# Performance work log

Hardware: AMD Instinct MI355X
Metric: run time of the kernel (lower is better)

The kernel has to match this reference:

```python
import jax, jax.numpy as jnp
import numpy as np

B, L, D = 1, 1024, 1024
NL = 4            # n_layers
N = 16            # d_state
DI = 2 * D        # d_inner (expand=2)
DTR = (D + 15) // 16  # dt_rank = ceil(d_model/16) = 64
K = 4             # depthwise conv kernel size
EPS = 1e-5


def setup_inputs() -> dict:
    key = jax.random.key(0)
    ks = jax.random.split(key, 8)
    s = lambda k, shp, sc: jax.random.normal(k, shp, jnp.float32) * sc
    x = s(ks[0], (B, L, D), 1.0)
    norm_w = jnp.ones((NL, D), jnp.float32)
    in_w = s(ks[1], (NL, 2 * DI, D), D ** -0.5)          # in_proj (no bias)
    conv_w = s(ks[2], (NL, DI, K), 0.5)                   # depthwise conv1d weight
    conv_b = s(ks[3], (NL, DI), 0.02)                     # conv1d bias
    xproj_w = s(ks[4], (NL, DTR + 2 * N, DI), DI ** -0.5) # x_proj (no bias)
    dt_w = s(ks[5], (NL, DI, DTR), DTR ** -0.5)           # dt_proj weight
    dt_b = jnp.full((NL, DI), 0.1, jnp.float32)           # dt_proj bias (positive-ish delta)
    A_log = jnp.log(jnp.tile(jnp.arange(1, N + 1, dtype=jnp.float32), (NL, DI, 1)))  # [NL, DI, N]
    D_skip = jnp.ones((NL, DI), jnp.float32)
    out_w = s(ks[6], (NL, D, DI), DI ** -0.5)             # out_proj (no bias)
    return dict(x=x, norm_w=norm_w, in_w=in_w, conv_w=conv_w, conv_b=conv_b,
                xproj_w=xproj_w, dt_w=dt_w, dt_b=dt_b, A_log=A_log,
                D_skip=D_skip, out_w=out_w)


def _rmsnorm(x, w):
    return x * jax.lax.rsqrt(jnp.mean(x * x, axis=-1, keepdims=True) + EPS) * w


def _causal_depthwise_conv(u, w, b):
    # u: [B, L, DI], w: [DI, K], b: [DI]; causal (left pad K-1)
    up = jnp.pad(u, ((0, 0), (K - 1, 0), (0, 0)))
    y = b
    for k in range(K):
        y = y + up[:, k:k + L, :] * w[:, k]
    return y


def _selective_scan(dA, dBu, C):
    # dA, dBu: [B, L, DI, N]; C: [B, L, N]
    def step(h, inp):
        a, bu, c = inp
        h = a * h + bu                       # [B, DI, N]
        y = jnp.einsum('bdn,bn->bd', h, c)   # [B, DI]
        return h, y
    h0 = jnp.zeros((dA.shape[0], DI, N), dA.dtype)
    _, ys = jax.lax.scan(step, h0, (dA.transpose(1, 0, 2, 3),
                                    dBu.transpose(1, 0, 2, 3),
                                    C.transpose(1, 0, 2)))
    return ys.transpose(1, 0, 2)             # [B, L, DI]


def _mamba_block(x, p):
    norm_w, in_w, conv_w, conv_b, xproj_w, dt_w, dt_b, A_log, D_skip, out_w = p
    xn = _rmsnorm(x, norm_w)
    xz = jnp.einsum('bld,ed->ble', xn, in_w)             # [B, L, 2*DI]
    u, z = jnp.split(xz, 2, axis=-1)
    u = jax.nn.silu(_causal_depthwise_conv(u, conv_w, conv_b))
    x_dbl = jnp.einsum('bld,ed->ble', u, xproj_w)        # [B, L, DTR+2N]
    dt_r, Bt, Ct = jnp.split(x_dbl, [DTR, DTR + N], axis=-1)
    delta = jax.nn.softplus(jnp.einsum('blr,dr->bld', dt_r, dt_w) + dt_b)  # [B, L, DI]
    A = -jnp.exp(A_log)                                  # [DI, N]
    dA = jnp.exp(delta[..., None] * A)                   # [B, L, DI, N]
    dBu = delta[..., None] * Bt[:, :, None, :] * u[..., None]
    y = _selective_scan(dA, dBu, Ct) + u * D_skip        # [B, L, DI]
    y = y * jax.nn.silu(z)
    return x + jnp.einsum('ble,de->bld', y, out_w)       # residual


def reference(x, norm_w, in_w, conv_w, conv_b, xproj_w, dt_w, dt_b, A_log, D_skip, out_w):
    params = (norm_w, in_w, conv_w, conv_b, xproj_w, dt_w, dt_b, A_log, D_skip, out_w)
    out, _ = jax.lax.scan(lambda h, p: (_mamba_block(h, p), None), x, params)
    return out
```

## Files before the change

### kernel.cpp

```cpp
#include <hip/hip_runtime.h>
#include <hip/hip_bf16.h>
#include <stdint.h>

#define L 1024
#define D 1024
#define NLAYER 4
#define NSTATE 16
#define DI 2048
#define DTR 64
#define KCONV 4
#define XD 96
#define NC 64
#define CT 16
#define KSPLIT 8

typedef __attribute__((ext_vector_type(8))) short short8;
typedef __attribute__((ext_vector_type(4))) float floatx4;

__device__ __forceinline__ float siluf(float x) { return x / (1.f + __expf(-x)); }

__device__ __forceinline__ unsigned short f2bf(float x) {
    __hip_bfloat16 b = __float2bfloat16(x);
    return *reinterpret_cast<unsigned short*>(&b);
}

#ifndef __has_builtin
#define __has_builtin(x) 0
#endif
#if __has_builtin(__builtin_amdgcn_global_load_lds)
#define HAVE_GLD 1
#define GLD(gp, lp) __builtin_amdgcn_global_load_lds(                                  \
    (const __attribute__((address_space(1))) void*)(gp),                               \
    (__attribute__((address_space(3))) void*)(lp), 16, 0, 0)
#endif

#define N_IN4  1048576
#define N_XP4  49152
#define N_DT4  32768
#define N_OUT4 524288
#define N_CVT4 (N_IN4 + N_XP4 + N_DT4 + N_OUT4)

__global__ __launch_bounds__(256) void cvt_layer_kernel(
    const float* __restrict__ in_w, const float* __restrict__ xp_w,
    const float* __restrict__ dt_w, const float* __restrict__ out_w,
    __hip_bfloat16* __restrict__ in_bf, __hip_bfloat16* __restrict__ xp_bf,
    __hip_bfloat16* __restrict__ dt_bf, __hip_bfloat16* __restrict__ out_bf) {
    int i = blockIdx.x * 256 + threadIdx.x;
    if (i >= N_CVT4) return;
    const float* src;
    __hip_bfloat16* dst;
    int off;
    if (i < N_IN4) { src = in_w; dst = in_bf; off = i; }
    else if (i < N_IN4 + N_XP4) { src = xp_w; dst = xp_bf; off = i - N_IN4; }
    else if (i < N_IN4 + N_XP4 + N_DT4) { src = dt_w; dst = dt_bf; off = i - N_IN4 - N_XP4; }
    else { src = out_w; dst = out_bf; off = i - N_IN4 - N_XP4 - N_DT4; }
    float4 v = ((const float4*)src)[off];
    ushort4 o;
    o.x = f2bf(v.x); o.y = f2bf(v.y); o.z = f2bf(v.z); o.w = f2bf(v.w);
    ((ushort4*)dst)[off] = o;
}

__global__ __launch_bounds__(256) void rmsnorm_kernel(const float* __restrict__ x,
                                                      const float* __restrict__ w,
                                                      __hip_bfloat16* __restrict__ out) {
    int row = blockIdx.x;
    const float* xr = x + (size_t)row * D;
    float v[4];
    float s = 0.f;
#pragma unroll
    for (int i = 0; i < 4; ++i) {
        v[i] = xr[threadIdx.x + i * 256];
        s += v[i] * v[i];
    }
#pragma unroll
    for (int off = 32; off > 0; off >>= 1) s += __shfl_xor(s, off, 64);
    __shared__ float red[4];
    int wave = threadIdx.x >> 6;
    if ((threadIdx.x & 63) == 0) red[wave] = s;
    __syncthreads();
    float tot = red[0] + red[1] + red[2] + red[3];
    float inv = rsqrtf(tot * (1.f / D) + 1e-5f);
#pragma unroll
    for (int i = 0; i < 4; ++i) {
        int c = threadIdx.x + i * 256;
        out[(size_t)row * D + c] = __float2bfloat16(v[i] * inv * w[c]);
    }
}

#define BM 128
#define BN 64
#define BK 32

template <int EPI>
__global__ __launch_bounds__(256, 2) void gemm_mfma(
    const __hip_bfloat16* __restrict__ A, int lda,
    const __hip_bfloat16* __restrict__ B, int ldb,
    float* __restrict__ C, int ldc, int Nvalid,
    int kchunk, long zstride,
    const float* __restrict__ bias, const float* __restrict__ resid) {
    __shared__ __align__(16) __hip_bfloat16 As[BM * BK];
    __shared__ __align__(16) __hip_bfloat16 Bs[BN * BK];
    int tid = threadIdx.x;
    int wave = tid >> 6, lane = tid & 63;
    int m0 = blockIdx.y * BM, n0 = blockIdx.x * BN;
    int k_lo = blockIdx.z * kchunk;
    int k_hi = k_lo + kchunk;
    C += (long)blockIdx.z * zstride;
    int wr = wave >> 1, wc = wave & 1;
    int srow = lane >> 2, scol = (lane & 3) * 8;
    int q = lane >> 4, r = lane & 15;

    floatx4 acc[4][2] = {};

    const __hip_bfloat16* gA = A + (long)(m0 + wave * 32 + srow) * lda + scol;
    const __hip_bfloat16* gB = B + (long)(n0 + wave * 16 + srow) * ldb + scol;
    __hip_bfloat16* lA0 = As + (wave * 32) * BK;
    __hip_bfloat16* lA1 = As + (wave * 32 + 16) * BK;
    __hip_bfloat16* lB  = Bs + (wave * 16) * BK;

    for (int k0 = k_lo; k0 < k_hi; k0 += BK) {
#ifdef HAVE_GLD
        GLD(gA + k0, lA0);
        GLD(gA + (long)16 * lda + k0, lA1);
        GLD(gB + k0, lB);
#else
        short8 a0 = *(const short8*)(gA + k0);
        short8 a1 = *(const short8*)(gA + (long)16 * lda + k0);
        short8 b0 = *(const short8*)(gB + k0);
        *(short8*)(lA0 + lane * 8) = a0;
        *(short8*)(lA1 + lane * 8) = a1;
        *(short8*)(lB + lane * 8) = b0;
#endif
        __syncthreads();
        const short* Ap = (const short*)As;
        const short* Bp = (const short*)Bs;
        short8 af[4], bfr[2];
#pragma unroll
        for (int i = 0; i < 4; ++i)
            af[i] = *(const short8*)(Ap + (wr * 64 + i * 16 + r) * BK + q * 8);
#pragma unroll
        for (int j = 0; j < 2; ++j)
            bfr[j] = *(const short8*)(Bp + (wc * 32 + j * 16 + r) * BK + q * 8);
#pragma unroll
        for (int i = 0; i < 4; ++i)
#pragma unroll
            for (int j = 0; j < 2; ++j)
                acc[i][j] = __builtin_amdgcn_mfma_f32_16x16x32_bf16(af[i], bfr[j], acc[i][j], 0, 0, 0);
        __syncthreads();
    }

#pragma unroll
    for (int i = 0; i < 4; ++i) {
        int mrow = m0 + wr * 64 + i * 16 + q * 4;
#pragma unroll
        for (int j = 0; j < 2; ++j) {
            int ncol = n0 + wc * 32 + j * 16 + r;
            if (ncol < Nvalid) {
#pragma unroll
                for (int rr = 0; rr < 4; ++rr) {
                    float v = acc[i][j][rr];
                    int m = mrow + rr;
                    if (EPI == 1) {
                        v += bias[ncol];
                        v = v > 20.f ? v : log1pf(__expf(v));
                    } else if (EPI == 2) {
                        v += resid[(long)m * ldc + ncol];
                    }
                    C[(long)m * ldc + ncol] = v;
                }
            }
        }
    }
}

__global__ __launch_bounds__(256) void conv_silu_kernel(const float* __restrict__ xz,
                                                        const float* __restrict__ cw,
                                                        const float* __restrict__ cb,
                                                        __hip_bfloat16* __restrict__ u) {
    int idx = blockIdx.x * 256 + threadIdx.x;
    int d = idx & (DI - 1);
    int t = idx >> 11;
    float acc = cb[d];
#pragma unroll
    for (int k = 0; k < KCONV; ++k) {
        int tk = t - (KCONV - 1) + k;
        if (tk >= 0) acc += xz[(size_t)tk * (2 * DI) + d] * cw[d * KCONV + k];
    }
    u[idx] = __float2bfloat16(siluf(acc));
}

__global__ __launch_bounds__(256) void xdbl_reduce_kernel(const float* __restrict__ part,
                                                          float* __restrict__ xdbl,
                                                          __hip_bfloat16* __restrict__ xdbl_bf) {
    int i = blockIdx.x * 256 + threadIdx.x;
    float s = 0.f;
#pragma unroll
    for (int sp = 0; sp < KSPLIT; ++sp) s += part[(long)sp * L * XD + i];
    xdbl[i] = s;
    xdbl_bf[i] = __float2bfloat16(s);
}

__global__ __launch_bounds__(256) void scanA_kernel(const float* __restrict__ delta,
                                                    const __hip_bfloat16* __restrict__ u,
                                                    const float* __restrict__ xdbl,
                                                    const float* __restrict__ Alog,
                                                    float* __restrict__ Ach,
                                                    float* __restrict__ Bch) {
    int d = blockIdx.x * 256 + threadIdx.x;
    int c = blockIdx.y;
    __shared__ __align__(16) float Bsh[CT * NSTATE];
    int tt0 = threadIdx.x >> 4, c0 = threadIdx.x & 15;
    Bsh[threadIdx.x] = xdbl[(size_t)(c * CT + tt0) * XD + DTR + c0];
    __syncthreads();

    float aval[NSTATE];
    const float4* Al4 = (const float4*)(Alog + (size_t)d * NSTATE);
#pragma unroll
    for (int n4 = 0; n4 < 4; ++n4) {
        float4 t = Al4[n4];
        aval[n4 * 4 + 0] = -__expf(t.x);
        aval[n4 * 4 + 1] = -__expf(t.y);
        aval[n4 * 4 + 2] = -__expf(t.z);
        aval[n4 * 4 + 3] = -__expf(t.w);
    }
    float h[NSTATE], ap[NSTATE];
#pragma unroll
    for (int n = 0; n < NSTATE; ++n) { h[n] = 0.f; ap[n] = 1.f; }

    for (int tt = 0; tt < CT; ++tt) {
        int t = c * CT + tt;
        float dl = delta[(size_t)t * DI + d];
        float uu = __bfloat162float(u[(size_t)t * DI + d]);
        float du = dl * uu;
        const float4* Bv = (const float4*)(Bsh + tt * NSTATE);
#pragma unroll
        for (int n4 = 0; n4 < 4; ++n4) {
            float4 b = Bv[n4];
            float bb[4] = {b.x, b.y, b.z, b.w};
#pragma unroll
            for (int k = 0; k < 4; ++k) {
                int n = n4 * 4 + k;
                float a = __expf(dl * aval[n]);
                h[n] = a * h[n] + du * bb[k];
                ap[n] *= a;
            }
        }
    }
    float4* Ao = (float4*)(Ach + ((size_t)c * DI + d) * NSTATE);
    float4* Bo = (float4*)(Bch + ((size_t)c * DI + d) * NSTATE);
#pragma unroll
    for (int n4 = 0; n4 < 4; ++n4) {
        Ao[n4] = make_float4(ap[n4 * 4], ap[n4 * 4 + 1], ap[n4 * 4 + 2], ap[n4 * 4 + 3]);
        Bo[n4] = make_float4(h[n4 * 4], h[n4 * 4 + 1], h[n4 * 4 + 2], h[n4 * 4 + 3]);
    }
}

__global__ __launch_bounds__(256) void scanB_kernel(float* __restrict__ Ach,
                                                    const float* __restrict__ Bch) {
    long i = blockIdx.x * 256 + threadIdx.x;
    const long S = (long)DI * NSTATE;
    float h = 0.f;
    for (int c = 0; c < NC; ++c) {
        float a = Ach[c * S + i];
        float b = Bch[c * S + i];
        Ach[c * S + i] = h;
        h = a * h + b;
    }
}

__global__ __launch_bounds__(256) void scanC_kernel(const float* __restrict__ delta,
                                                    const __hip_bfloat16* __restrict__ u,
                                                    const float* __restrict__ xdbl,
                                                    const float* __restrict__ Alog,
                                                    const float* __restrict__ Hin,
                                                    const float* __restrict__ xz,
                                                    const float* __restrict__ Dskip,
                                                    __hip_bfloat16* __restrict__ yg) {
    int d = blockIdx.x * 256 + threadIdx.x;
    int c = blockIdx.y;
    __shared__ __align__(16) float Bsh[CT * NSTATE];
    __shared__ __align__(16) float Csh[CT * NSTATE];
    int tt0 = threadIdx.x >> 4, c0 = threadIdx.x & 15;
    Bsh[threadIdx.x] = xdbl[(size_t)(c * CT + tt0) * XD + DTR + c0];
    Csh[threadIdx.x] = xdbl[(size_t)(c * CT + tt0) * XD + DTR + NSTATE + c0];
    __syncthreads();

    float aval[NSTATE];
    const float4* Al4 = (const float4*)(Alog + (size_t)d * NSTATE);
#pragma unroll
    for (int n4 = 0; n4 < 4; ++n4) {
        float4 t = Al4[n4];
        aval[n4 * 4 + 0] = -__expf(t.x);
        aval[n4 * 4 + 1] = -__expf(t.y);
        aval[n4 * 4 + 2] = -__expf(t.z);
        aval[n4 * 4 + 3] = -__expf(t.w);
    }
    float h[NSTATE];
    const float4* Hi = (const float4*)(Hin + ((size_t)c * DI + d) * NSTATE);
#pragma unroll
    for (int n4 = 0; n4 < 4; ++n4) {
        float4 t = Hi[n4];
        h[n4 * 4 + 0] = t.x; h[n4 * 4 + 1] = t.y; h[n4 * 4 + 2] = t.z; h[n4 * 4 + 3] = t.w;
    }
    float dsk = Dskip[d];

    for (int tt = 0; tt < CT; ++tt) {
        int t = c * CT + tt;
        float dl = delta[(size_t)t * DI + d];
        float uu = __bfloat162float(u[(size_t)t * DI + d]);
        float du = dl * uu;
        const float4* Bv = (const float4*)(Bsh + tt * NSTATE);
        const float4* Cv = (const float4*)(Csh + tt * NSTATE);
        float y = 0.f;
#pragma unroll
        for (int n4 = 0; n4 < 4; ++n4) {
            float4 b = Bv[n4];
            float4 cc = Cv[n4];
            float bb[4] = {b.x, b.y, b.z, b.w};
            float cv[4] = {cc.x, cc.y, cc.z, cc.w};
#pragma unroll
            for (int k = 0; k < 4; ++k) {
                int n = n4 * 4 + k;
                float a = __expf(dl * aval[n]);
                h[n] = a * h[n] + du * bb[k];
                y += h[n] * cv[k];
            }
        }
        float z = xz[(size_t)t * (2 * DI) + DI + d];
        yg[(size_t)t * DI + d] = __float2bfloat16((y + uu * dsk) * siluf(z));
    }
}

extern "C" void kernel_launch(void* const* d_in, const int* in_sizes, int n_in,
                              void* d_out, int out_size, void* d_ws, size_t ws_size,
                              hipStream_t stream) {
    const float* x      = (const float*)d_in[0];
    const float* norm_w = (const float*)d_in[1];
    const float* in_w   = (const float*)d_in[2];
    const float* conv_w = (const float*)d_in[3];
    const float* conv_b = (const float*)d_in[4];
    const float* xproj_w= (const float*)d_in[5];
    const float* dt_w   = (const float*)d_in[6];
    const float* dt_b   = (const float*)d_in[7];
    const float* A_log  = (const float*)d_in[8];
    const float* D_skip = (const float*)d_in[9];
    const float* out_w  = (const float*)d_in[10];
    float* out = (float*)d_out;

    uint8_t* wp = (uint8_t*)d_ws;
    auto alloc = [&](size_t bytes) {
        uint8_t* p = wp;
        wp += (bytes + 255) & ~(size_t)255;
        return p;
    };
    __hip_bfloat16* w_in_bf  = (__hip_bfloat16*)alloc((size_t)4096 * 1024 * 2);
    __hip_bfloat16* w_xp_bf  = (__hip_bfloat16*)alloc((size_t)128 * 2048 * 2);
    __hip_bfloat16* w_dt_bf  = (__hip_bfloat16*)alloc((size_t)2048 * 64 * 2);
    __hip_bfloat16* w_out_bf = (__hip_bfloat16*)alloc((size_t)1024 * 2048 * 2);
    __hip_bfloat16* xn_bf    = (__hip_bfloat16*)alloc((size_t)L * D * 2);
    float*          xz       = (float*)alloc((size_t)L * 2 * DI * 4);
    __hip_bfloat16* u_bf     = (__hip_bfloat16*)alloc((size_t)L * DI * 2);
    float*          xdbl     = (float*)alloc((size_t)L * XD * 4);
    __hip_bfloat16* xdbl_bf  = (__hip_bfloat16*)alloc((size_t)L * XD * 2);
    float*          part     = (float*)alloc((size_t)KSPLIT * L * XD * 4);
    float*          delta    = (float*)alloc((size_t)L * DI * 4);
    __hip_bfloat16* yg_bf    = (__hip_bfloat16*)alloc((size_t)L * DI * 2);
    float*          Ach      = (float*)alloc((size_t)NC * DI * NSTATE * 4);
    float*          Bch      = (float*)alloc((size_t)NC * DI * NSTATE * 4);

    for (int l = 0; l < NLAYER; ++l) {
        const float* xin = (l == 0) ? x : out;

        cvt_layer_kernel<<<(N_CVT4 + 255) / 256, 256, 0, stream>>>(
            in_w + (size_t)l * 4096 * 1024, xproj_w + (size_t)l * 96 * 2048,
            dt_w + (size_t)l * 2048 * 64, out_w + (size_t)l * 1024 * 2048,
            w_in_bf, w_xp_bf, w_dt_bf, w_out_bf);

        rmsnorm_kernel<<<L, 256, 0, stream>>>(xin, norm_w + (size_t)l * D, xn_bf);

        gemm_mfma<0><<<dim3(4096 / BN, L / BM, 1), 256, 0, stream>>>(
            xn_bf, D, w_in_bf, D, xz, 4096, 4096, D, 0, nullptr, nullptr);

        conv_silu_kernel<<<L * DI / 256, 256, 0, stream>>>(
            xz, conv_w + (size_t)l * DI * KCONV, conv_b + (size_t)l * DI, u_bf);

        gemm_mfma<0><<<dim3(2, L / BM, KSPLIT), 256, 0, stream>>>(
            u_bf, DI, w_xp_bf, DI, part, XD, XD, DI / KSPLIT, (long)L * XD, nullptr, nullptr);
        xdbl_reduce_kernel<<<(L * XD) / 256, 256, 0, stream>>>(part, xdbl, xdbl_bf);

        gemm_mfma<1><<<dim3(2048 / BN, L / BM, 1), 256, 0, stream>>>(
            xdbl_bf, XD, w_dt_bf, DTR, delta, DI, DI, DTR, 0,
            dt_b + (size_t)l * DI, nullptr);

        scanA_kernel<<<dim3(DI / 256, NC), 256, 0, stream>>>(
            delta, u_bf, xdbl, A_log + (size_t)l * DI * NSTATE, Ach, Bch);
        scanB_kernel<<<(DI * NSTATE) / 256, 256, 0, stream>>>(Ach, Bch);
        scanC_kernel<<<dim3(DI / 256, NC), 256, 0, stream>>>(
            delta, u_bf, xdbl, A_log + (size_t)l * DI * NSTATE, Ach, xz,
            D_skip + (size_t)l * DI, yg_bf);

        gemm_mfma<2><<<dim3(1024 / BN, L / BM, 1), 256, 0, stream>>>(
            yg_bf, DI, w_out_bf, DI, out, D, D, DI, 0, nullptr, xin);
    }
}
```

Before: 682.5 us.

## Widen GEMM N-tile to 128 and convert all layer weights in one launch

Templates the MFMA GEMM on its N tile width and uses 128-wide tiles for the in_proj, x_proj and dt_proj GEMMs, which raises arithmetic intensity per loaded A tile. The per-layer weight conversion kernels are merged into one launch before the layer loop, writing into per-layer bf16 buffers. The x_proj split-K factor goes from 8 to 16 so the grid stays populated after the tile widening. The cost is a larger bf16 workspace holding every layer's weights and more accumulator registers per thread, which may lower occupancy.

Result: slower. 729.2 us (+6.8%).

```diff
diff --git a/kernel.cpp b/kernel.cpp
--- a/kernel.cpp
+++ b/kernel.cpp
@@ -12,7 +12,7 @@
 #define XD 96
 #define NC 64
 #define CT 16
-#define KSPLIT 8
+#define KSPLIT 16
 
 typedef __attribute__((ext_vector_type(8))) short short8;
 typedef __attribute__((ext_vector_type(4))) float floatx4;
@@ -40,20 +40,31 @@
 #define N_OUT4 524288
 #define N_CVT4 (N_IN4 + N_XP4 + N_DT4 + N_OUT4)
 
-__global__ __launch_bounds__(256) void cvt_layer_kernel(
+__global__ __launch_bounds__(256) void cvt_all_kernel(
     const float* __restrict__ in_w, const float* __restrict__ xp_w,
     const float* __restrict__ dt_w, const float* __restrict__ out_w,
     __hip_bfloat16* __restrict__ in_bf, __hip_bfloat16* __restrict__ xp_bf,
     __hip_bfloat16* __restrict__ dt_bf, __hip_bfloat16* __restrict__ out_bf) {
-    int i = blockIdx.x * 256 + threadIdx.x;
-    if (i >= N_CVT4) return;
+    int gi = blockIdx.x * 256 + threadIdx.x;
+    if (gi >= NLAYER * N_CVT4) return;
+    int layer = gi / N_CVT4;
+    int i = gi - layer * N_CVT4;
     const float* src;
     __hip_bfloat16* dst;
     int off;
-    if (i < N_IN4) { src = in_w; dst = in_bf; off = i; }
-    else if (i < N_IN4 + N_XP4) { src = xp_w; dst = xp_bf; off = i - N_IN4; }
-    else if (i < N_IN4 + N_XP4 + N_DT4) { src = dt_w; dst = dt_bf; off = i - N_IN4 - N_XP4; }
-    else { src = out_w; dst = out_bf; off = i - N_IN4 - N_XP4 - N_DT4; }
+    if (i < N_IN4) {
+        src = in_w + (size_t)layer * 4096 * 1024;
+        dst = in_bf + (size_t)layer * 4096 * 1024; off = i;
+    } else if (i < N_IN4 + N_XP4) {
+        src = xp_w + (size_t)layer * 96 * 2048;
+        dst = xp_bf + (size_t)layer * 128 * 2048; off = i - N_IN4;
+    } else if (i < N_IN4 + N_XP4 + N_DT4) {
+        src = dt_w + (size_t)layer * 2048 * 64;
+        dst = dt_bf + (size_t)layer * 2048 * 64; off = i - N_IN4 - N_XP4;
+    } else {
+        src = out_w + (size_t)layer * 1024 * 2048;
+        dst = out_bf + (size_t)layer * 1024 * 2048; off = i - N_IN4 - N_XP4 - N_DT4;
+    }
     float4 v = ((const float4*)src)[off];
     ushort4 o;
     o.x = f2bf(v.x); o.y = f2bf(v.y); o.z = f2bf(v.z); o.w = f2bf(v.w);
@@ -87,22 +98,22 @@
     }
 }
 
-#define BM 128
-#define BN 64
 #define BK 32
 
-template <int EPI>
+template <int TN, int EPI>
 __global__ __launch_bounds__(256, 2) void gemm_mfma(
     const __hip_bfloat16* __restrict__ A, int lda,
     const __hip_bfloat16* __restrict__ B, int ldb,
     float* __restrict__ C, int ldc, int Nvalid,
     int kchunk, long zstride,
     const float* __restrict__ bias, const float* __restrict__ resid) {
-    __shared__ __align__(16) __hip_bfloat16 As[BM * BK];
-    __shared__ __align__(16) __hip_bfloat16 Bs[BN * BK];
+    constexpr int NF = TN / 32;
+    constexpr int WCOLS = TN / 2;
+    __shared__ __align__(16) __hip_bfloat16 As[128 * BK];
+    __shared__ __align__(16) __hip_bfloat16 Bs[TN * BK];
     int tid = threadIdx.x;
     int wave = tid >> 6, lane = tid & 63;
-    int m0 = blockIdx.y * BM, n0 = blockIdx.x * BN;
+    int m0 = blockIdx.y * 128, n0 = blockIdx.x * TN;
     int k_lo = blockIdx.z * kchunk;
     int k_hi = k_lo + kchunk;
     C += (long)blockIdx.z * zstride;
@@ -110,41 +121,52 @@
     int srow = lane >> 2, scol = (lane & 3) * 8;
     int q = lane >> 4, r = lane & 15;
 
-    floatx4 acc[4][2] = {};
-
-    const __hip_bfloat16* gA = A + (long)(m0 + wave * 32 + srow) * lda + scol;
-    const __hip_bfloat16* gB = B + (long)(n0 + wave * 16 + srow) * ldb + scol;
+    floatx4 acc[4][NF] = {};
+
+    const __hip_bfloat16* gA0 = A + (long)(m0 + wave * 32 + srow) * lda + scol;
+    const __hip_bfloat16* gA1 = gA0 + (long)16 * lda;
     __hip_bfloat16* lA0 = As + (wave * 32) * BK;
     __hip_bfloat16* lA1 = As + (wave * 32 + 16) * BK;
-    __hip_bfloat16* lB  = Bs + (wave * 16) * BK;
+    const __hip_bfloat16* gB0;
+    const __hip_bfloat16* gB1 = nullptr;
+    __hip_bfloat16* lB0;
+    __hip_bfloat16* lB1 = nullptr;
+    if (TN == 128) {
+        gB0 = B + (long)(n0 + wave * 32 + srow) * ldb + scol;
+        gB1 = gB0 + (long)16 * ldb;
+        lB0 = Bs + (wave * 32) * BK;
+        lB1 = Bs + (wave * 32 + 16) * BK;
+    } else {
+        gB0 = B + (long)(n0 + wave * 16 + srow) * ldb + scol;
+        lB0 = Bs + (wave * 16) * BK;
+    }
 
     for (int k0 = k_lo; k0 < k_hi; k0 += BK) {
 #ifdef HAVE_GLD
-        GLD(gA + k0, lA0);
-        GLD(gA + (long)16 * lda + k0, lA1);
-        GLD(gB + k0, lB);
+        GLD(gA0 + k0, lA0);
+        GLD(gA1 + k0, lA1);
+        GLD(gB0 + k0, lB0);
+        if (TN == 128) GLD(gB1 + k0, lB1);
 #else
-        short8 a0 = *(const short8*)(gA + k0);
-        short8 a1 = *(const short8*)(gA + (long)16 * lda + k0);
-        short8 b0 = *(const short8*)(gB + k0);
-        *(short8*)(lA0 + lane * 8) = a0;
-        *(short8*)(lA1 + lane * 8) = a1;
-        *(short8*)(lB + lane * 8) = b0;
+        *(short8*)(lA0 + lane * 8) = *(const short8*)(gA0 + k0 - scol + (lane & 3) * 8);
+        *(short8*)(lA1 + lane * 8) = *(const short8*)(gA1 + k0 - scol + (lane & 3) * 8);
+        *(short8*)(lB0 + lane * 8) = *(const short8*)(gB0 + k0 - scol + (lane & 3) * 8);
+        if (TN == 128) *(short8*)(lB1 + lane * 8) = *(const short8*)(gB1 + k0 - scol + (lane & 3) * 8);
 #endif
         __syncthreads();
         const short* Ap = (const short*)As;
         const short* Bp = (const short*)Bs;
-        short8 af[4], bfr[2];
+        short8 af[4], bfr[NF];
 #pragma unroll
         for (int i = 0; i < 4; ++i)
             af[i] = *(const short8*)(Ap + (wr * 64 + i * 16 + r) * BK + q * 8);
 #pragma unroll
-        for (int j = 0; j < 2; ++j)
-            bfr[j] = *(const short8*)(Bp + (wc * 32 + j * 16 + r) * BK + q * 8);
+        for (int j = 0; j < NF; ++j)
+            bfr[j] = *(const short8*)(Bp + (wc * WCOLS + j * 16 + r) * BK + q * 8);
 #pragma unroll
         for (int i = 0; i < 4; ++i)
 #pragma unroll
-            for (int j = 0; j < 2; ++j)
+            for (int j = 0; j < NF; ++j)
                 acc[i][j] = __builtin_amdgcn_mfma_f32_16x16x32_bf16(af[i], bfr[j], acc[i][j], 0, 0, 0);
         __syncthreads();
     }
@@ -153,8 +175,8 @@
     for (int i = 0; i < 4; ++i) {
         int mrow = m0 + wr * 64 + i * 16 + q * 4;
 #pragma unroll
-        for (int j = 0; j < 2; ++j) {
-            int ncol = n0 + wc * 32 + j * 16 + r;
+        for (int j = 0; j < NF; ++j) {
+            int ncol = n0 + wc * WCOLS + j * 16 + r;
             if (ncol < Nvalid) {
 #pragma unroll
                 for (int rr = 0; rr < 4; ++rr) {
@@ -353,10 +375,10 @@
         wp += (bytes + 255) & ~(size_t)255;
         return p;
     };
-    __hip_bfloat16* w_in_bf  = (__hip_bfloat16*)alloc((size_t)4096 * 1024 * 2);
-    __hip_bfloat16* w_xp_bf  = (__hip_bfloat16*)alloc((size_t)128 * 2048 * 2);
-    __hip_bfloat16* w_dt_bf  = (__hip_bfloat16*)alloc((size_t)2048 * 64 * 2);
-    __hip_bfloat16* w_out_bf = (__hip_bfloat16*)alloc((size_t)1024 * 2048 * 2);
+    __hip_bfloat16* w_in_bf  = (__hip_bfloat16*)alloc((size_t)NLAYER * 4096 * 1024 * 2);
+    __hip_bfloat16* w_xp_bf  = (__hip_bfloat16*)alloc((size_t)NLAYER * 128 * 2048 * 2);
+    __hip_bfloat16* w_dt_bf  = (__hip_bfloat16*)alloc((size_t)NLAYER * 2048 * 64 * 2);
+    __hip_bfloat16* w_out_bf = (__hip_bfloat16*)alloc((size_t)NLAYER * 1024 * 2048 * 2);
     __hip_bfloat16* xn_bf    = (__hip_bfloat16*)alloc((size_t)L * D * 2);
     float*          xz       = (float*)alloc((size_t)L * 2 * DI * 4);
     __hip_bfloat16* u_bf     = (__hip_bfloat16*)alloc((size_t)L * DI * 2);
@@ -368,28 +390,30 @@
     float*          Ach      = (float*)alloc((size_t)NC * DI * NSTATE * 4);
     float*          Bch      = (float*)alloc((size_t)NC * DI * NSTATE * 4);
 
+    cvt_all_kernel<<<(NLAYER * N_CVT4 + 255) / 256, 256, 0, stream>>>(
+        in_w, xproj_w, dt_w, out_w, w_in_bf, w_xp_bf, w_dt_bf, w_out_bf);
+
     for (int l = 0; l < NLAYER; ++l) {
         const float* xin = (l == 0) ? x : out;
-
-        cvt_layer_kernel<<<(N_CVT4 + 255) / 256, 256, 0, stream>>>(
-            in_w + (size_t)l * 4096 * 1024, xproj_w + (size_t)l * 96 * 2048,
-            dt_w + (size_t)l * 2048 * 64, out_w + (size_t)l * 1024 * 2048,
-            w_in_bf, w_xp_bf, w_dt_bf, w_out_bf);
+        const __hip_bfloat16* wi = w_in_bf + (size_t)l * 4096 * 1024;
+        const __hip_bfloat16* wx = w_xp_bf + (size_t)l * 128 * 2048;
+        const __hip_bfloat16* wd = w_dt_bf + (size_t)l * 2048 * 64;
+        const __hip_bfloat16* wo = w_out_bf + (size_t)l * 1024 * 2048;
 
         rmsnorm_kernel<<<L, 256, 0, stream>>>(xin, norm_w + (size_t)l * D, xn_bf);
 
-        gemm_mfma<0><<<dim3(4096 / BN, L / BM, 1), 256, 0, stream>>>(
-            xn_bf, D, w_in_bf, D, xz, 4096, 4096, D, 0, nullptr, nullptr);
+        gemm_mfma<128, 0><<<dim3(4096 / 128, L / 128, 1), 256, 0, stream>>>(
+            xn_bf, D, wi, D, xz, 4096, 4096, D, 0, nullptr, nullptr);
 
         conv_silu_kernel<<<L * DI / 256, 256, 0, stream>>>(
             xz, conv_w + (size_t)l * DI * KCONV, conv_b + (size_t)l * DI, u_bf);
 
-        gemm_mfma<0><<<dim3(2, L / BM, KSPLIT), 256, 0, stream>>>(
-            u_bf, DI, w_xp_bf, DI, part, XD, XD, DI / KSPLIT, (long)L * XD, nullptr, nullptr);
+        gemm_mfma<128, 0><<<dim3(1, L / 128, KSPLIT), 256, 0, stream>>>(
+            u_bf, DI, wx, DI, part, XD, XD, DI / KSPLIT, (long)L * XD, nullptr, nullptr);
         xdbl_reduce_kernel<<<(L * XD) / 256, 256, 0, stream>>>(part, xdbl, xdbl_bf);
 
-        gemm_mfma<1><<<dim3(2048 / BN, L / BM, 1), 256, 0, stream>>>(
-            xdbl_bf, XD, w_dt_bf, DTR, delta, DI, DI, DTR, 0,
+        gemm_mfma<128, 1><<<dim3(2048 / 128, L / 128, 1), 256, 0, stream>>>(
+            xdbl_bf, XD, wd, DTR, delta, DI, DI, DTR, 0,
             dt_b + (size_t)l * DI, nullptr);
 
         scanA_kernel<<<dim3(DI / 256, NC), 256, 0, stream>>>(
@@ -399,7 +423,7 @@
             delta, u_bf, xdbl, A_log + (size_t)l * DI * NSTATE, Ach, xz,
             D_skip + (size_t)l * DI, yg_bf);
 
-        gemm_mfma<2><<<dim3(1024 / BN, L / BM, 1), 256, 0, stream>>>(
-            yg_bf, DI, w_out_bf, DI, out, D, D, DI, 0, nullptr, xin);
-    }
-}
+        gemm_mfma<64, 2><<<dim3(1024 / 64, L / 128, 1), 256, 0, stream>>>(
+            yg_bf, DI, wo, DI, out, D, D, DI, 0, nullptr, xin);
+    }
+}
```

## Fuse weight conversion, RMSNorm and split-K reduce into GEMM staging with double buffering

Applied to the files above, without the earlier changes.

Removes the separate fp32-to-bf16 weight conversion, RMSNorm and x_dbl reduction kernels. The GEMM now reads fp32 weights and activations directly, converting them to bf16 while staging into LDS. The norm weight is folded into B, the per-row inverse RMS is applied in the epilogue, and the split-K partials are summed while loading A for the dt GEMM and inside the scan kernels. LDS is double-buffered so the next tile loads during the current MFMA, which drops the async global-to-LDS path for weights. In exchange, the out and in projection GEMMs re-read fp32 weights from every M tile (twice the bytes of bf16), and the partials are reduced redundantly in several places.

After: 856.3 us. 25.5% more time.

```diff
diff --git a/kernel.cpp b/kernel.cpp
--- a/kernel.cpp
+++ b/kernel.cpp
@@ -13,6 +13,7 @@
 #define NC 64
 #define CT 16
 #define KSPLIT 8
+#define BK 32
 
 typedef __attribute__((ext_vector_type(8))) short short8;
 typedef __attribute__((ext_vector_type(4))) float floatx4;
@@ -22,6 +23,15 @@
 __device__ __forceinline__ unsigned short f2bf(float x) {
     __hip_bfloat16 b = __float2bfloat16(x);
     return *reinterpret_cast<unsigned short*>(&b);
+}
+
+__device__ __forceinline__ short8 pack8(floatx4 a, floatx4 b) {
+    short8 o;
+    o[0] = (short)f2bf(a.x); o[1] = (short)f2bf(a.y);
+    o[2] = (short)f2bf(a.z); o[3] = (short)f2bf(a.w);
+    o[4] = (short)f2bf(b.x); o[5] = (short)f2bf(b.y);
+    o[6] = (short)f2bf(b.z); o[7] = (short)f2bf(b.w);
+    return o;
 }
 
 #ifndef __has_builtin
@@ -34,77 +44,21 @@
     (__attribute__((address_space(3))) void*)(lp), 16, 0, 0)
 #endif
 
-#define N_IN4  1048576
-#define N_XP4  49152
-#define N_DT4  32768
-#define N_OUT4 524288
-#define N_CVT4 (N_IN4 + N_XP4 + N_DT4 + N_OUT4)
-
-__global__ __launch_bounds__(256) void cvt_layer_kernel(
-    const float* __restrict__ in_w, const float* __restrict__ xp_w,
-    const float* __restrict__ dt_w, const float* __restrict__ out_w,
-    __hip_bfloat16* __restrict__ in_bf, __hip_bfloat16* __restrict__ xp_bf,
-    __hip_bfloat16* __restrict__ dt_bf, __hip_bfloat16* __restrict__ out_bf) {
-    int i = blockIdx.x * 256 + threadIdx.x;
-    if (i >= N_CVT4) return;
-    const float* src;
-    __hip_bfloat16* dst;
-    int off;
-    if (i < N_IN4) { src = in_w; dst = in_bf; off = i; }
-    else if (i < N_IN4 + N_XP4) { src = xp_w; dst = xp_bf; off = i - N_IN4; }
-    else if (i < N_IN4 + N_XP4 + N_DT4) { src = dt_w; dst = dt_bf; off = i - N_IN4 - N_XP4; }
-    else { src = out_w; dst = out_bf; off = i - N_IN4 - N_XP4 - N_DT4; }
-    float4 v = ((const float4*)src)[off];
-    ushort4 o;
-    o.x = f2bf(v.x); o.y = f2bf(v.y); o.z = f2bf(v.z); o.w = f2bf(v.w);
-    ((ushort4*)dst)[off] = o;
-}
-
-__global__ __launch_bounds__(256) void rmsnorm_kernel(const float* __restrict__ x,
-                                                      const float* __restrict__ w,
-                                                      __hip_bfloat16* __restrict__ out) {
-    int row = blockIdx.x;
-    const float* xr = x + (size_t)row * D;
-    float v[4];
-    float s = 0.f;
-#pragma unroll
-    for (int i = 0; i < 4; ++i) {
-        v[i] = xr[threadIdx.x + i * 256];
-        s += v[i] * v[i];
-    }
-#pragma unroll
-    for (int off = 32; off > 0; off >>= 1) s += __shfl_xor(s, off, 64);
-    __shared__ float red[4];
-    int wave = threadIdx.x >> 6;
-    if ((threadIdx.x & 63) == 0) red[wave] = s;
-    __syncthreads();
-    float tot = red[0] + red[1] + red[2] + red[3];
-    float inv = rsqrtf(tot * (1.f / D) + 1e-5f);
-#pragma unroll
-    for (int i = 0; i < 4; ++i) {
-        int c = threadIdx.x + i * 256;
-        out[(size_t)row * D + c] = __float2bfloat16(v[i] * inv * w[c]);
-    }
-}
-
-#define BM 128
-#define BN 64
-#define BK 32
-
-template <int EPI>
+template <int EPI, int ASRC, bool BNW>
 __global__ __launch_bounds__(256, 2) void gemm_mfma(
-    const __hip_bfloat16* __restrict__ A, int lda,
-    const __hip_bfloat16* __restrict__ B, int ldb,
+    const void* __restrict__ Ax, int lda,
+    const float* __restrict__ Bw, int ldb, int Brows,
     float* __restrict__ C, int ldc, int Nvalid,
     int kchunk, long zstride,
-    const float* __restrict__ bias, const float* __restrict__ resid) {
-    __shared__ __align__(16) __hip_bfloat16 As[BM * BK];
-    __shared__ __align__(16) __hip_bfloat16 Bs[BN * BK];
+    const float* __restrict__ bias, const float* __restrict__ resid,
+    const float* __restrict__ nw, long pstride) {
+    __shared__ __align__(16) __hip_bfloat16 As[2][128 * BK];
+    __shared__ __align__(16) __hip_bfloat16 Bs[2][64 * BK];
+    __shared__ float normS[128];
     int tid = threadIdx.x;
     int wave = tid >> 6, lane = tid & 63;
-    int m0 = blockIdx.y * BM, n0 = blockIdx.x * BN;
-    int k_lo = blockIdx.z * kchunk;
-    int k_hi = k_lo + kchunk;
+    int m0 = blockIdx.y * 128, n0 = blockIdx.x * 64;
+    int k_lo = blockIdx.z * kchunk, k_hi = k_lo + kchunk;
     C += (long)blockIdx.z * zstride;
     int wr = wave >> 1, wc = wave & 1;
     int srow = lane >> 2, scol = (lane & 3) * 8;
@@ -112,28 +66,76 @@
 
     floatx4 acc[4][2] = {};
 
-    const __hip_bfloat16* gA = A + (long)(m0 + wave * 32 + srow) * lda + scol;
-    const __hip_bfloat16* gB = B + (long)(n0 + wave * 16 + srow) * ldb + scol;
-    __hip_bfloat16* lA0 = As + (wave * 32) * BK;
-    __hip_bfloat16* lA1 = As + (wave * 32 + 16) * BK;
-    __hip_bfloat16* lB  = Bs + (wave * 16) * BK;
-
+    const __hip_bfloat16* gA0b = nullptr;
+    const __hip_bfloat16* gA1b = nullptr;
+    const float* gA0f = nullptr;
+    const float* gA1f = nullptr;
+    if (ASRC == 0) {
+        gA0b = (const __hip_bfloat16*)Ax + (long)(m0 + wave * 32 + srow) * lda + scol;
+        gA1b = gA0b + (long)16 * lda;
+    } else {
+        gA0f = (const float*)Ax + (long)(m0 + wave * 32 + srow) * lda + scol;
+        gA1f = gA0f + (long)16 * lda;
+    }
+    int brow = n0 + wave * 16 + srow;
+    const float* gB = Bw + (long)brow * ldb + scol;
+    bool bok = brow < Brows;
+
+    float ss0 = 0.f, ss1 = 0.f;
+
+    auto stage = [&](int k0, int p) {
+        if (ASRC == 0) {
+#ifdef HAVE_GLD
+            GLD(gA0b + k0, &As[p][(wave * 32) * BK]);
+            GLD(gA1b + k0, &As[p][(wave * 32 + 16) * BK]);
+#else
+            *(short8*)(&As[p][(wave * 32 + srow) * BK + scol]) = *(const short8*)(gA0b + k0);
+            *(short8*)(&As[p][(wave * 32 + 16 + srow) * BK + scol]) = *(const short8*)(gA1b + k0);
+#endif
+        } else if (ASRC == 1) {
+            floatx4 v0 = *(const floatx4*)(gA0f + k0);
+            floatx4 v1 = *(const floatx4*)(gA0f + k0 + 4);
+            floatx4 w0 = *(const floatx4*)(gA1f + k0);
+            floatx4 w1 = *(const floatx4*)(gA1f + k0 + 4);
+            ss0 += v0.x * v0.x + v0.y * v0.y + v0.z * v0.z + v0.w * v0.w
+                 + v1.x * v1.x + v1.y * v1.y + v1.z * v1.z + v1.w * v1.w;
+            ss1 += w0.x * w0.x + w0.y * w0.y + w0.z * w0.z + w0.w * w0.w
+                 + w1.x * w1.x + w1.y * w1.y + w1.z * w1.z + w1.w * w1.w;
+            *(short8*)(&As[p][(wave * 32 + srow) * BK + scol]) = pack8(v0, v1);
+            *(short8*)(&As[p][(wave * 32 + 16 + srow) * BK + scol]) = pack8(w0, w1);
+        } else {
+            floatx4 v0 = {0.f, 0.f, 0.f, 0.f}, v1 = v0, w0 = v0, w1 = v0;
+#pragma unroll
+            for (int sp = 0; sp < KSPLIT; ++sp) {
+                const float* p0 = gA0f + sp * pstride + k0;
+                const float* p1 = gA1f + sp * pstride + k0;
+                v0 += *(const floatx4*)(p0);
+                v1 += *(const floatx4*)(p0 + 4);
+                w0 += *(const floatx4*)(p1);
+                w1 += *(const floatx4*)(p1 + 4);
+            }
+            *(short8*)(&As[p][(wave * 32 + srow) * BK + scol]) = pack8(v0, v1);
+            *(short8*)(&As[p][(wave * 32 + 16 + srow) * BK + scol]) = pack8(w0, w1);
+        }
+        floatx4 b0 = {0.f, 0.f, 0.f, 0.f}, b1 = b0;
+        if (bok) {
+            b0 = *(const floatx4*)(gB + k0);
+            b1 = *(const floatx4*)(gB + k0 + 4);
+        }
+        if (BNW) {
+            b0 *= *(const floatx4*)(nw + k0 + scol);
+            b1 *= *(const floatx4*)(nw + k0 + scol + 4);
+        }
+        *(short8*)(&Bs[p][(wave * 16 + srow) * BK + scol]) = pack8(b0, b1);
+    };
+
+    stage(k_lo, 0);
+    int p = 0;
     for (int k0 = k_lo; k0 < k_hi; k0 += BK) {
-#ifdef HAVE_GLD
-        GLD(gA + k0, lA0);
-        GLD(gA + (long)16 * lda + k0, lA1);
-        GLD(gB + k0, lB);
-#else
-        short8 a0 = *(const short8*)(gA + k0);
-        short8 a1 = *(const short8*)(gA + (long)16 * lda + k0);
-        short8 b0 = *(const short8*)(gB + k0);
-        *(short8*)(lA0 + lane * 8) = a0;
-        *(short8*)(lA1 + lane * 8) = a1;
-        *(short8*)(lB + lane * 8) = b0;
-#endif
         __syncthreads();
-        const short* Ap = (const short*)As;
-        const short* Bp = (const short*)Bs;
+        if (k0 + BK < k_hi) stage(k0 + BK, p ^ 1);
+        const short* Ap = (const short*)As[p];
+        const short* Bp = (const short*)Bs[p];
         short8 af[4], bfr[2];
 #pragma unroll
         for (int i = 0; i < 4; ++i)
@@ -146,12 +148,22 @@
 #pragma unroll
             for (int j = 0; j < 2; ++j)
                 acc[i][j] = __builtin_amdgcn_mfma_f32_16x16x32_bf16(af[i], bfr[j], acc[i][j], 0, 0, 0);
+        p ^= 1;
+    }
+
+    if (ASRC == 1) {
+        ss0 += __shfl_xor(ss0, 1); ss0 += __shfl_xor(ss0, 2);
+        ss1 += __shfl_xor(ss1, 1); ss1 += __shfl_xor(ss1, 2);
+        if ((lane & 3) == 0) {
+            normS[wave * 32 + srow] = ss0;
+            normS[wave * 32 + 16 + srow] = ss1;
+        }
         __syncthreads();
     }
 
 #pragma unroll
     for (int i = 0; i < 4; ++i) {
-        int mrow = m0 + wr * 64 + i * 16 + q * 4;
+        int lr0 = wr * 64 + i * 16 + q * 4;
 #pragma unroll
         for (int j = 0; j < 2; ++j) {
             int ncol = n0 + wc * 32 + j * 16 + r;
@@ -159,7 +171,10 @@
 #pragma unroll
                 for (int rr = 0; rr < 4; ++rr) {
                     float v = acc[i][j][rr];
-                    int m = mrow + rr;
+                    int lr = lr0 + rr;
+                    int m = m0 + lr;
+                    if (ASRC == 1)
+                        v *= rsqrtf(normS[lr] * (1.f / 1024.f) + 1e-5f);
                     if (EPI == 1) {
                         v += bias[ncol];
                         v = v > 20.f ? v : log1pf(__expf(v));
@@ -189,20 +204,9 @@
     u[idx] = __float2bfloat16(siluf(acc));
 }
 
-__global__ __launch_bounds__(256) void xdbl_reduce_kernel(const float* __restrict__ part,
-                                                          float* __restrict__ xdbl,
-                                                          __hip_bfloat16* __restrict__ xdbl_bf) {
-    int i = blockIdx.x * 256 + threadIdx.x;
-    float s = 0.f;
-#pragma unroll
-    for (int sp = 0; sp < KSPLIT; ++sp) s += part[(long)sp * L * XD + i];
-    xdbl[i] = s;
-    xdbl_bf[i] = __float2bfloat16(s);
-}
-
 __global__ __launch_bounds__(256) void scanA_kernel(const float* __restrict__ delta,
                                                     const __hip_bfloat16* __restrict__ u,
-                                                    const float* __restrict__ xdbl,
+                                                    const float* __restrict__ part,
                                                     const float* __restrict__ Alog,
                                                     float* __restrict__ Ach,
                                                     float* __restrict__ Bch) {
@@ -210,7 +214,13 @@
     int c = blockIdx.y;
     __shared__ __align__(16) float Bsh[CT * NSTATE];
     int tt0 = threadIdx.x >> 4, c0 = threadIdx.x & 15;
-    Bsh[threadIdx.x] = xdbl[(size_t)(c * CT + tt0) * XD + DTR + c0];
+    {
+        float s = 0.f;
+        size_t base = (size_t)(c * CT + tt0) * XD + DTR + c0;
+#pragma unroll
+        for (int sp = 0; sp < KSPLIT; ++sp) s += part[(size_t)sp * L * XD + base];
+        Bsh[threadIdx.x] = s;
+    }
     __syncthreads();
 
     float aval[NSTATE];
@@ -270,7 +280,7 @@
 
 __global__ __launch_bounds__(256) void scanC_kernel(const float* __restrict__ delta,
                                                     const __hip_bfloat16* __restrict__ u,
-                                                    const float* __restrict__ xdbl,
+                                                    const float* __restrict__ part,
                                                     const float* __restrict__ Alog,
                                                     const float* __restrict__ Hin,
                                                     const float* __restrict__ xz,
@@ -281,8 +291,17 @@
     __shared__ __align__(16) float Bsh[CT * NSTATE];
     __shared__ __align__(16) float Csh[CT * NSTATE];
     int tt0 = threadIdx.x >> 4, c0 = threadIdx.x & 15;
-    Bsh[threadIdx.x] = xdbl[(size_t)(c * CT + tt0) * XD + DTR + c0];
-    Csh[threadIdx.x] = xdbl[(size_t)(c * CT + tt0) * XD + DTR + NSTATE + c0];
+    {
+        float sb = 0.f, sc = 0.f;
+        size_t base = (size_t)(c * CT + tt0) * XD + DTR + c0;
+#pragma unroll
+        for (int sp = 0; sp < KSPLIT; ++sp) {
+            sb += part[(size_t)sp * L * XD + base];
+            sc += part[(size_t)sp * L * XD + base + NSTATE];
+        }
+        Bsh[threadIdx.x] = sb;
+        Csh[threadIdx.x] = sc;
+    }
     __syncthreads();
 
     float aval[NSTATE];
@@ -353,53 +372,41 @@
         wp += (bytes + 255) & ~(size_t)255;
         return p;
     };
-    __hip_bfloat16* w_in_bf  = (__hip_bfloat16*)alloc((size_t)4096 * 1024 * 2);
-    __hip_bfloat16* w_xp_bf  = (__hip_bfloat16*)alloc((size_t)128 * 2048 * 2);
-    __hip_bfloat16* w_dt_bf  = (__hip_bfloat16*)alloc((size_t)2048 * 64 * 2);
-    __hip_bfloat16* w_out_bf = (__hip_bfloat16*)alloc((size_t)1024 * 2048 * 2);
-    __hip_bfloat16* xn_bf    = (__hip_bfloat16*)alloc((size_t)L * D * 2);
-    float*          xz       = (float*)alloc((size_t)L * 2 * DI * 4);
-    __hip_bfloat16* u_bf     = (__hip_bfloat16*)alloc((size_t)L * DI * 2);
-    float*          xdbl     = (float*)alloc((size_t)L * XD * 4);
-    __hip_bfloat16* xdbl_bf  = (__hip_bfloat16*)alloc((size_t)L * XD * 2);
-    float*          part     = (float*)alloc((size_t)KSPLIT * L * XD * 4);
-    float*          delta    = (float*)alloc((size_t)L * DI * 4);
-    __hip_bfloat16* yg_bf    = (__hip_bfloat16*)alloc((size_t)L * DI * 2);
-    float*          Ach      = (float*)alloc((size_t)NC * DI * NSTATE * 4);
-    float*          Bch      = (float*)alloc((size_t)NC * DI * NSTATE * 4);
+    float*          xz    = (float*)alloc((size_t)L * 2 * DI * 4);
+    __hip_bfloat16* u_bf  = (__hip_bfloat16*)alloc((size_t)L * DI * 2);
+    float*          part  = (float*)alloc((size_t)KSPLIT * L * XD * 4);
+    float*          delta = (float*)alloc((size_t)L * DI * 4);
+    __hip_bfloat16* yg_bf = (__hip_bfloat16*)alloc((size_t)L * DI * 2);
+    float*          Ach   = (float*)alloc((size_t)NC * DI * NSTATE * 4);
+    float*          Bch   = (float*)alloc((size_t)NC * DI * NSTATE * 4);
 
     for (int l = 0; l < NLAYER; ++l) {
         const float* xin = (l == 0) ? x : out;
 
-        cvt_layer_kernel<<<(N_CVT4 + 255) / 256, 256, 0, stream>>>(
-            in_w + (size_t)l * 4096 * 1024, xproj_w + (size_t)l * 96 * 2048,
-            dt_w + (size_t)l * 2048 * 64, out_w + (size_t)l * 1024 * 2048,
-            w_in_bf, w_xp_bf, w_dt_bf, w_out_bf);
-
-        rmsnorm_kernel<<<L, 256, 0, stream>>>(xin, norm_w + (size_t)l * D, xn_bf);
-
-        gemm_mfma<0><<<dim3(4096 / BN, L / BM, 1), 256, 0, stream>>>(
-            xn_bf, D, w_in_bf, D, xz, 4096, 4096, D, 0, nullptr, nullptr);
+        gemm_mfma<0, 1, true><<<dim3(4096 / 64, L / 128, 1), 256, 0, stream>>>(
+            xin, D, in_w + (size_t)l * 4096 * 1024, D, 4096,
+            xz, 4096, 4096, D, 0, nullptr, nullptr, norm_w + (size_t)l * D, 0);
 
         conv_silu_kernel<<<L * DI / 256, 256, 0, stream>>>(
             xz, conv_w + (size_t)l * DI * KCONV, conv_b + (size_t)l * DI, u_bf);
 
-        gemm_mfma<0><<<dim3(2, L / BM, KSPLIT), 256, 0, stream>>>(
-            u_bf, DI, w_xp_bf, DI, part, XD, XD, DI / KSPLIT, (long)L * XD, nullptr, nullptr);
-        xdbl_reduce_kernel<<<(L * XD) / 256, 256, 0, stream>>>(part, xdbl, xdbl_bf);
-
-        gemm_mfma<1><<<dim3(2048 / BN, L / BM, 1), 256, 0, stream>>>(
-            xdbl_bf, XD, w_dt_bf, DTR, delta, DI, DI, DTR, 0,
-            dt_b + (size_t)l * DI, nullptr);
+        gemm_mfma<0, 0, false><<<dim3(2, L / 128, KSPLIT), 256, 0, stream>>>(
+            u_bf, DI, xproj_w + (size_t)l * 96 * 2048, DI, 96,
+            part, XD, XD, DI / KSPLIT, (long)L * XD, nullptr, nullptr, nullptr, 0);
+
+        gemm_mfma<1, 2, false><<<dim3(2048 / 64, L / 128, 1), 256, 0, stream>>>(
+            part, XD, dt_w + (size_t)l * 2048 * 64, DTR, 2048,
+            delta, DI, DI, DTR, 0, dt_b + (size_t)l * DI, nullptr, nullptr, (long)L * XD);
 
         scanA_kernel<<<dim3(DI / 256, NC), 256, 0, stream>>>(
-            delta, u_bf, xdbl, A_log + (size_t)l * DI * NSTATE, Ach, Bch);
+            delta, u_bf, part, A_log + (size_t)l * DI * NSTATE, Ach, Bch);
         scanB_kernel<<<(DI * NSTATE) / 256, 256, 0, stream>>>(Ach, Bch);
         scanC_kernel<<<dim3(DI / 256, NC), 256, 0, stream>>>(
-            delta, u_bf, xdbl, A_log + (size_t)l * DI * NSTATE, Ach, xz,
+            delta, u_bf, part, A_log + (size_t)l * DI * NSTATE, Ach, xz,
             D_skip + (size_t)l * DI, yg_bf);
 
-        gemm_mfma<2><<<dim3(1024 / BN, L / BM, 1), 256, 0, stream>>>(
-            yg_bf, DI, w_out_bf, DI, out, D, D, DI, 0, nullptr, xin);
-    }
-}
+        gemm_mfma<2, 0, false><<<dim3(1024 / 64, L / 128, 1), 256, 0, stream>>>(
+            yg_bf, DI, out_w + (size_t)l * 1024 * 2048, DI, 1024,
+            out, D, D, DI, 0, nullptr, xin, nullptr, 0);
+    }
+}
```
